# Kernel tuning notes

Hardware: AMD Instinct MI355X
Metric: run time of the kernel (lower is better)

## Reference

```python
import jax, jax.numpy as jnp
import numpy as np

EMBED_DIM = 1024
NUM_HEADS = 16
D_K = EMBED_DIM // NUM_HEADS
FFN_DIM = 4096
EPS = 1e-5


def _linear_params(key, fan_in, fan_out):
    kw, kb = jax.random.split(key)
    bound = 1.0 / np.sqrt(fan_in)
    W = jax.random.uniform(kw, (fan_out, fan_in), jnp.float32, -bound, bound)
    b = jax.random.uniform(kb, (fan_out,), jnp.float32, -bound, bound)
    return W, b


def setup_inputs() -> dict:
    key = jax.random.key(0)
    ks = jax.random.split(key, 8)
    x = jax.random.normal(ks[0], (2, 2048, EMBED_DIM), jnp.float32)
    Wq, bq = _linear_params(ks[1], EMBED_DIM, EMBED_DIM)
    Wk, bk = _linear_params(ks[2], EMBED_DIM, EMBED_DIM)
    Wv, bv = _linear_params(ks[3], EMBED_DIM, EMBED_DIM)
    Wo, bo = _linear_params(ks[4], EMBED_DIM, EMBED_DIM)
    W1, b1 = _linear_params(ks[5], EMBED_DIM, FFN_DIM)
    W2, b2 = _linear_params(ks[6], FFN_DIM, EMBED_DIM)
    g1 = jnp.ones((EMBED_DIM,), jnp.float32)
    be1 = jnp.zeros((EMBED_DIM,), jnp.float32)
    g2 = jnp.ones((EMBED_DIM,), jnp.float32)
    be2 = jnp.zeros((EMBED_DIM,), jnp.float32)
    return {"x": x, "Wq": Wq, "bq": bq, "Wk": Wk, "bk": bk, "Wv": Wv, "bv": bv,
            "Wo": Wo, "bo": bo, "W1": W1, "b1": b1, "W2": W2, "b2": b2,
            "g1": g1, "be1": be1, "g2": g2, "be2": be2}


def _layernorm(x, g, b):
    mu = jnp.mean(x, axis=-1, keepdims=True)
    var = jnp.var(x, axis=-1, keepdims=True)
    return (x - mu) * jax.lax.rsqrt(var + EPS) * g + b


def reference(x, Wq, bq, Wk, bk, Wv, bv, Wo, bo, W1, b1, W2, b2, g1, be1, g2, be2):
    B, S, _ = x.shape
    h = _layernorm(x, g1, be1)
    # qkv projections -> [B, H, S, d_k]
    def split_heads(t):
        return t.reshape(B, S, NUM_HEADS, D_K).transpose(0, 2, 1, 3)
    q = split_heads(h @ Wq.T + bq)
    k = split_heads(h @ Wk.T + bk)
    v = split_heads(h @ Wv.T + bv)
    scores = jnp.einsum('bhqd,bhkd->bhqk', q, k) / np.sqrt(D_K).astype(np.float32)
    attn = jax.nn.softmax(scores, axis=-1)
    out = jnp.einsum('bhqk,bhkd->bhqd', attn, v)
    out = out.transpose(0, 2, 1, 3).reshape(B, S, EMBED_DIM)
    attn_out = out @ Wo.T + bo
    x = x + attn_out
    h2 = _layernorm(x, g2, be2)
    ffn = jax.nn.relu(h2 @ W1.T + b1) @ W2.T + b2
    return x + ffn
```

## Files before the change

### kernel.cpp

```cpp
#include <hip/hip_runtime.h>

typedef __attribute__((ext_vector_type(8))) short short8;
typedef __attribute__((ext_vector_type(4))) float f32x4;
typedef __attribute__((ext_vector_type(4))) unsigned short us4;

#define MFMA_BF16(a, b, c) __builtin_amdgcn_mfma_f32_16x16x32_bf16((a), (b), (c), 0, 0, 0)

__device__ __forceinline__ unsigned short f2bf(float f) {
  union { float f; unsigned int u; } x; x.f = f;
  unsigned int r = x.u + 0x7FFFu + ((x.u >> 16) & 1u);
  return (unsigned short)(r >> 16);
}
__device__ __forceinline__ float bf2f(unsigned short b) {
  union { float f; unsigned int u; } x; x.u = ((unsigned int)b) << 16;
  return x.f;
}

typedef __attribute__((address_space(3))) unsigned int lds_uint;
typedef const __attribute__((address_space(1))) unsigned int gbl_uint;

__device__ __forceinline__ void gload_lds16(const void* g, void* l) {
  __builtin_amdgcn_global_load_lds((gbl_uint*)g, (lds_uint*)l, 16, 0, 0);
}

__device__ __forceinline__ short8 lds_swz_read(const unsigned short* base, int row, int colbyte) {
  return *(const short8*)((const char*)base + row * 128 + (colbyte ^ ((row & 7) << 4)));
}

__global__ __launch_bounds__(256) void cvt_ln(const float* __restrict__ Wq,
                                              const float* __restrict__ Wk,
                                              const float* __restrict__ Wv,
                                              const float* __restrict__ Wo,
                                              const float* __restrict__ W1,
                                              const float* __restrict__ W2,
                                              unsigned short* __restrict__ Wqkv_b,
                                              unsigned short* __restrict__ Wo_b,
                                              unsigned short* __restrict__ W1_b,
                                              unsigned short* __restrict__ W2_b,
                                              const float* __restrict__ x,
                                              const float* __restrict__ g,
                                              const float* __restrict__ be,
                                              unsigned short* __restrict__ lnout) {
  const int b = blockIdx.x;
  const int t = threadIdx.x;
  __shared__ float red[8];
  if (b < 12288) {
    const float* src;
    unsigned short* dst;
    int off;
    if (b < 1024)      { src = Wq; dst = Wqkv_b;           off = b; }
    else if (b < 2048) { src = Wk; dst = Wqkv_b + 1048576; off = b - 1024; }
    else if (b < 3072) { src = Wv; dst = Wqkv_b + 2097152; off = b - 2048; }
    else if (b < 4096) { src = Wo; dst = Wo_b;             off = b - 3072; }
    else if (b < 8192) { src = W1; dst = W1_b;             off = b - 4096; }
    else               { src = W2; dst = W2_b;             off = b - 8192; }
    const int i = off * 256 + t;
    const float4 v = ((const float4*)src)[i];
    us4 o;
    o.x = f2bf(v.x); o.y = f2bf(v.y); o.z = f2bf(v.z); o.w = f2bf(v.w);
    ((us4*)dst)[i] = o;
    return;
  }
  const int row = b - 12288;
  const float4 v = ((const float4*)(x + (size_t)row * 1024))[t];
  float s = v.x + v.y + v.z + v.w;
  float s2 = v.x * v.x + v.y * v.y + v.z * v.z + v.w * v.w;
#pragma unroll
  for (int d = 1; d < 64; d <<= 1) {
    s += __shfl_xor(s, d);
    s2 += __shfl_xor(s2, d);
  }
  const int wid = t >> 6, lane = t & 63;
  if (lane == 0) { red[wid] = s; red[4 + wid] = s2; }
  __syncthreads();
  s = red[0] + red[1] + red[2] + red[3];
  s2 = red[4] + red[5] + red[6] + red[7];
  const float mu = s * (1.0f / 1024.0f);
  const float var = s2 * (1.0f / 1024.0f) - mu * mu;
  const float rstd = rsqrtf(var + 1e-5f);
  const float4 gv = ((const float4*)g)[t];
  const float4 bv = ((const float4*)be)[t];
  us4 o;
  o.x = f2bf((v.x - mu) * rstd * gv.x + bv.x);
  o.y = f2bf((v.y - mu) * rstd * gv.y + bv.y);
  o.z = f2bf((v.z - mu) * rstd * gv.z + bv.z);
  o.w = f2bf((v.w - mu) * rstd * gv.w + bv.w);
  ((us4*)(lnout + (size_t)row * 1024))[t] = o;
}

__global__ __launch_bounds__(256) void ln_kernel(const float* __restrict__ x,
                                                 const float* __restrict__ g,
                                                 const float* __restrict__ be,
                                                 unsigned short* __restrict__ out) {
  const int row = blockIdx.x;
  const int t = threadIdx.x;
  const float4 v = ((const float4*)(x + (size_t)row * 1024))[t];
  float s = v.x + v.y + v.z + v.w;
  float s2 = v.x * v.x + v.y * v.y + v.z * v.z + v.w * v.w;
#pragma unroll
  for (int d = 1; d < 64; d <<= 1) {
    s += __shfl_xor(s, d);
    s2 += __shfl_xor(s2, d);
  }
  __shared__ float red[8];
  const int wid = t >> 6, lane = t & 63;
  if (lane == 0) { red[wid] = s; red[4 + wid] = s2; }
  __syncthreads();
  s = red[0] + red[1] + red[2] + red[3];
  s2 = red[4] + red[5] + red[6] + red[7];
  const float mu = s * (1.0f / 1024.0f);
  const float var = s2 * (1.0f / 1024.0f) - mu * mu;
  const float rstd = rsqrtf(var + 1e-5f);
  const float4 gv = ((const float4*)g)[t];
  const float4 bv = ((const float4*)be)[t];
  us4 o;
  o.x = f2bf((v.x - mu) * rstd * gv.x + bv.x);
  o.y = f2bf((v.y - mu) * rstd * gv.y + bv.y);
  o.z = f2bf((v.z - mu) * rstd * gv.z + bv.z);
  o.w = f2bf((v.w - mu) * rstd * gv.w + bv.w);
  ((us4*)(out + (size_t)row * 1024))[t] = o;
}

__global__ __launch_bounds__(256) void ffn2_reduce(float* __restrict__ out,
                                                   const float* __restrict__ p1,
                                                   const float* __restrict__ x1,
                                                   const float* __restrict__ b2) {
  const int row = blockIdx.x, t = threadIdx.x;
  const size_t i = (size_t)row * 256 + t;
  float4 v = ((const float4*)out)[i];
  const float4 a = ((const float4*)p1)[i];
  const float4 c = ((const float4*)x1)[i];
  const float4 b = ((const float4*)b2)[t];
  v.x += a.x + c.x + b.x; v.y += a.y + c.y + b.y;
  v.z += a.z + c.z + b.z; v.w += a.w + c.w + b.w;
  ((float4*)out)[i] = v;
}

template <int BN, int EPI, int MINW = 2>
__global__ __launch_bounds__(256, MINW) void gemm_bf16(const unsigned short* __restrict__ A,
                                                       const unsigned short* __restrict__ B,
                                                       const float* __restrict__ bias,
                                                       const float* __restrict__ biasK,
                                                       const float* __restrict__ biasV,
                                                       const float* __restrict__ res,
                                                       void* __restrict__ outp,
                                                       int M, int N, int K,
                                                       int gx, int gy, int kspl) {
  constexpr int WN = (BN == 128) ? 2 : 1;
  constexpr int WROWS = 128 / (4 / WN);
  constexpr int MW = WROWS / 16;
  constexpr int NW = (BN / WN) / 16;
  constexpr int BCH = BN / 32;
  constexpr int LOADS = 4 + BCH;

  __shared__ __align__(16) unsigned short As[2][128 * 64];
  __shared__ __align__(16) unsigned short Bs[2][BN * 64];

  const int nwg = gridDim.x;
  const int id2 = ((int)blockIdx.x & 7) * (nwg >> 3) + ((int)blockIdx.x >> 3);
  const int bx = id2 % gx;
  const int byz = id2 / gx;
  const int by = byz % gy;
  const int bz = byz / gy;

  const int wid = threadIdx.x >> 6;
  const int lane = threadIdx.x & 63;
  const int lr = lane & 15, lg = lane >> 4;
  const int row0 = by * 128;
  const int col0 = bx * BN;
  const int k0 = bz * kspl;
  const int wm = (wid / WN) * WROWS;
  const int wn = (wid % WN) * (BN / WN);

  const int scol = ((lane & 7) ^ ((lane >> 3) & 7)) * 8;

  auto stage = [&](int buf, int kt) {
#pragma unroll
    for (int i = 0; i < 4; ++i) {
      const int r = wid * 32 + i * 8;
      gload_lds16(A + (size_t)(row0 + r + (lane >> 3)) * K + kt + scol,
                  (void*)&As[buf][r * 64]);
    }
#pragma unroll
    for (int i = 0; i < BCH; ++i) {
      const int r = wid * (8 * BCH) + i * 8;
      gload_lds16(B + (size_t)(col0 + r + (lane >> 3)) * K + kt + scol,
                  (void*)&Bs[buf][r * 64]);
    }
  };

  f32x4 acc[MW][NW];
#pragma unroll
  for (int m = 0; m < MW; ++m)
#pragma unroll
    for (int n = 0; n < NW; ++n) acc[m][n] = (f32x4){0.f, 0.f, 0.f, 0.f};

  auto mma = [&](int buf) {
#pragma unroll
    for (int kk = 0; kk < 64; kk += 32) {
      const int colbyte = kk * 2 + lg * 16;
      short8 av[MW], bv[NW];
#pragma unroll
      for (int m = 0; m < MW; ++m)
        av[m] = lds_swz_read(&As[buf][0], wm + m * 16 + lr, colbyte);
#pragma unroll
      for (int n = 0; n < NW; ++n)
        bv[n] = lds_swz_read(&Bs[buf][0], wn + n * 16 + lr, colbyte);
#pragma unroll
      for (int m = 0; m < MW; ++m)
#pragma unroll
        for (int n = 0; n < NW; ++n) acc[m][n] = MFMA_BF16(av[m], bv[n], acc[m][n]);
    }
  };

  stage(0, k0);
  stage(1, k0 + 64);
  const int ktend = k0 + kspl;
  int cur = 0;
  for (int kt = k0; kt < ktend - 64; kt += 64) {
    asm volatile("s_waitcnt vmcnt(%0)" ::"i"(LOADS) : "memory");
    __builtin_amdgcn_s_barrier();
    __builtin_amdgcn_sched_barrier(0);
    mma(cur);
    __builtin_amdgcn_s_barrier();
    if (kt + 128 < ktend) stage(cur, kt + 128);
    cur ^= 1;
  }
  asm volatile("s_waitcnt vmcnt(0)" ::: "memory");
  __builtin_amdgcn_s_barrier();
  __builtin_amdgcn_sched_barrier(0);
  mma(cur);

#pragma unroll
  for (int m = 0; m < MW; ++m) {
#pragma unroll
    for (int n = 0; n < NW; ++n) {
#pragma unroll
      for (int r = 0; r < 4; ++r) {
        const int row = row0 + wm + m * 16 + lg * 4 + r;
        const int col = col0 + wn + n * 16 + lr;
        if constexpr (EPI == 0) {
          const int which = col >> 10, c = col & 1023;
          const float* bp = (which == 0) ? bias : (which == 1) ? biasK : biasV;
          const float v = acc[m][n][r] + bp[c];
          const size_t idx = (size_t)which * 4194304 +
              ((((size_t)(row >> 11)) * 16 + (c >> 6)) * 2048 + (row & 2047)) * 64 + (c & 63);
          ((unsigned short*)outp)[idx] = f2bf(v);
        } else if constexpr (EPI == 1) {
          const float v = acc[m][n][r] + bias[col];
          ((unsigned short*)outp)[(size_t)row * N + col] = f2bf(fmaxf(v, 0.f));
        } else {
          const float v = acc[m][n][r] + bias[col];
          ((float*)outp)[(size_t)row * N + col] = v + res[(size_t)row * N + col];
        }
      }
    }
  }
}

template <int BM, int BN, int EPI>
__global__ __launch_bounds__(512, 2) void gemm256(const unsigned short* __restrict__ A,
                                                  const unsigned short* __restrict__ B,
                                                  const float* __restrict__ bias,
                                                  float* __restrict__ part,
                                                  void* __restrict__ outp,
                                                  int M, int N, int K,
                                                  int gx, int gy, int kspl) {
  constexpr int MW = BM / 32;
  constexpr int NW = BN / 64;
  constexpr int A_ISS = BM / 64;
  constexpr int B_ISS = BN / 64;
  constexpr int LOADS = A_ISS + B_ISS;

  __shared__ __align__(16) unsigned short As[2][BM * 64];
  __shared__ __align__(16) unsigned short Bs[2][BN * 64];

  const int nwg = gridDim.x;
  const int id2 = ((int)blockIdx.x & 7) * (nwg >> 3) + ((int)blockIdx.x >> 3);
  const int bx = id2 % gx;
  const int byz = id2 / gx;
  const int by = byz % gy;
  const int bz = byz / gy;

  const int wid = threadIdx.x >> 6;
  const int lane = threadIdx.x & 63;
  const int lr = lane & 15, lg = lane >> 4;
  const int wr = wid >> 2, wc = wid & 3;
  const int row0 = by * BM;
  const int col0 = bx * BN;
  const int k0 = bz * kspl;
  const int wm = wr * (BM / 2);
  const int wn = wc * (BN / 4);

  const int scol = ((lane & 7) ^ ((lane >> 3) & 7)) * 8;

  auto stage = [&](int buf, int kt) {
#pragma unroll
    for (int i = 0; i < A_ISS; ++i) {
      const int r = wid * 8 + i * 64;
      gload_lds16(A + (size_t)(row0 + r + (lane >> 3)) * K + kt + scol,
                  (void*)&As[buf][r * 64]);
    }
#pragma unroll
    for (int i = 0; i < B_ISS; ++i) {
      const int r = wid * 8 + i * 64;
      gload_lds16(B + (size_t)(col0 + r + (lane >> 3)) * K + kt + scol,
                  (void*)&Bs[buf][r * 64]);
    }
  };

  f32x4 acc[MW][NW];
#pragma unroll
  for (int m = 0; m < MW; ++m)
#pragma unroll
    for (int n = 0; n < NW; ++n) acc[m][n] = (f32x4){0.f, 0.f, 0.f, 0.f};

  auto mma = [&](int buf) {
#pragma unroll
    for (int kk = 0; kk < 64; kk += 32) {
      const int colbyte = kk * 2 + lg * 16;
      short8 av[MW], bv[NW];
#pragma unroll
      for (int m = 0; m < MW; ++m)
        av[m] = lds_swz_read(&As[buf][0], wm + m * 16 + lr, colbyte);
#pragma unroll
      for (int n = 0; n < NW; ++n)
        bv[n] = lds_swz_read(&Bs[buf][0], wn + n * 16 + lr, colbyte);
#pragma unroll
      for (int m = 0; m < MW; ++m)
#pragma unroll
        for (int n = 0; n < NW; ++n) acc[m][n] = MFMA_BF16(av[m], bv[n], acc[m][n]);
    }
  };

  stage(0, k0);
  stage(1, k0 + 64);
  const int ktend = k0 + kspl;
  int cur = 0;
  for (int kt = k0; kt < ktend - 64; kt += 64) {
    asm volatile("s_waitcnt vmcnt(%0)" ::"i"(LOADS) : "memory");
    __builtin_amdgcn_s_barrier();
    __builtin_amdgcn_sched_barrier(0);
    mma(cur);
    __builtin_amdgcn_s_barrier();
    if (kt + 128 < ktend) stage(cur, kt + 128);
    cur ^= 1;
  }
  asm volatile("s_waitcnt vmcnt(0)" ::: "memory");
  __builtin_amdgcn_s_barrier();
  __builtin_amdgcn_sched_barrier(0);
  mma(cur);

#pragma unroll
  for (int m = 0; m < MW; ++m) {
#pragma unroll
    for (int n = 0; n < NW; ++n) {
#pragma unroll
      for (int r = 0; r < 4; ++r) {
        const int row = row0 + wm + m * 16 + lg * 4 + r;
        const int col = col0 + wn + n * 16 + lr;
        if constexpr (EPI == 1) {
          const float v = acc[m][n][r] + bias[col];
          ((unsigned short*)outp)[(size_t)row * N + col] = f2bf(fmaxf(v, 0.f));
        } else {
          float* dst = bz ? part : (float*)outp;
          dst[(size_t)row * N + col] = acc[m][n][r];
        }
      }
    }
  }
}

__global__ __launch_bounds__(256, 2) void attn_kernel(const unsigned short* __restrict__ q,
                                                      const unsigned short* __restrict__ k,
                                                      const unsigned short* __restrict__ v,
                                                      unsigned short* __restrict__ o) {
  const int bh = blockIdx.x;
  const int q0 = blockIdx.y * 128;
  const unsigned short* qh = q + (size_t)bh * 2048 * 64;
  const unsigned short* kh = k + (size_t)bh * 2048 * 64;
  const unsigned short* vh = v + (size_t)bh * 2048 * 64;
  const int wid = threadIdx.x >> 6, lane = threadIdx.x & 63;
  const int lr = lane & 15, lg = lane >> 4;
  const int qw = q0 + wid * 32;

  __shared__ __align__(16) unsigned short Vt[2][64 * 64];
  __shared__ __align__(16) unsigned short Ps[4][32 * 64];

  constexpr float CS = 0.125f * 1.4426950408889634f;
  short8 qf[2][2];
#pragma unroll
  for (int m = 0; m < 2; ++m)
#pragma unroll
    for (int kk = 0; kk < 2; ++kk) {
      short8 t = *(const short8*)&qh[(size_t)(qw + m * 16 + lr) * 64 + kk * 32 + lg * 8];
#pragma unroll
      for (int j = 0; j < 8; ++j) t[j] = (short)f2bf(bf2f((unsigned short)t[j]) * CS);
      qf[m][kk] = t;
    }

  f32x4 po[2][4];
  float lrun[2][4];
#pragma unroll
  for (int m = 0; m < 2; ++m) {
#pragma unroll
    for (int n = 0; n < 4; ++n) po[m][n] = (f32x4){0.f, 0.f, 0.f, 0.f};
#pragma unroll
    for (int r = 0; r < 4; ++r) lrun[m][r] = 0.f;
  }

  const int vd0 = wid * 16;
  const unsigned short* const vsrc = vh + (size_t)lane * 64 + vd0;
  const int sig2 = ((lane & 15) << 3) | ((lane >> 4) << 1);
  char* const PsB = (char*)&Ps[wid][0];

  short8 kfA[4][2], kfB[4][2], vA0, vA1, vB0, vB1;

#define LOAD_K(KF, kt)                                                                   \
  {                                                                                      \
    _Pragma("unroll") for (int n = 0; n < 4; ++n) _Pragma("unroll") for (int kk = 0;     \
                                                                         kk < 2; ++kk)  \
        KF[n][kk] =                                                                      \
        *(const short8*)&kh[(size_t)((kt) + n * 16 + lr) * 64 + kk * 32 + lg * 8];       \
  }
#define LOAD_V(V0, V1, kt)                                                               \
  {                                                                                      \
    V0 = *(const short8*)(vsrc + (size_t)(kt) * 64);                                     \
    V1 = *(const short8*)(vsrc + (size_t)(kt) * 64 + 8);                                 \
  }

  LOAD_K(kfA, 0)
  LOAD_V(vA0, vA1, 0)

#define STEP(KC, KN, VC0, VC1, VN0, VN1, BUF, t)                                         \
  {                                                                                      \
    char* const VtB = (char*)&Vt[BUF][0];                                                \
    _Pragma("unroll") for (int j = 0; j < 8; ++j) {                                      \
      const int row = vd0 + j;                                                           \
      *(unsigned short*)(VtB + row * 128 + (sig2 ^ ((row & 7) << 4))) =                  \
          (unsigned short)VC0[j];                                                        \
      const int row2 = vd0 + 8 + j;                                                      \
      *(unsigned short*)(VtB + row2 * 128 + (sig2 ^ ((row2 & 7) << 4))) =                \
          (unsigned short)VC1[j];                                                        \
    }                                                                                    \
    f32x4 sc[2][4];                                                                      \
    _Pragma("unroll") for (int m = 0; m < 2; ++m) _Pragma("unroll") for (int n = 0;      \
                                                                         n < 4; ++n)    \
        sc[m][n] = (f32x4){0.f, 0.f, 0.f, 0.f};                                          \
    __builtin_amdgcn_s_setprio(1);                                                       \
    _Pragma("unroll") for (int kk = 0; kk < 2; ++kk)                                     \
        _Pragma("unroll") for (int m = 0; m < 2; ++m)                                    \
        _Pragma("unroll") for (int n = 0; n < 4; ++n)                                    \
        sc[m][n] = MFMA_BF16(qf[m][kk], KC[n][kk], sc[m][n]);                            \
    __builtin_amdgcn_s_setprio(0);                                                       \
    const int ktn = ((t) + 1 < 32) ? ((t) + 1) * 64 : 0;                                 \
    LOAD_V(VN0, VN1, ktn)                                                                \
    LOAD_K(KN, ktn)                                                                      \
    _Pragma("unroll") for (int m = 0; m < 2; ++m)                                        \
        _Pragma("unroll") for (int r = 0; r < 4; ++r) {                                  \
      const float p0 = __builtin_amdgcn_exp2f(sc[m][0][r]);                              \
      const float p1 = __builtin_amdgcn_exp2f(sc[m][1][r]);                              \
      const float p2 = __builtin_amdgcn_exp2f(sc[m][2][r]);                              \
      const float p3 = __builtin_amdgcn_exp2f(sc[m][3][r]);                              \
      lrun[m][r] += (p0 + p1) + (p2 + p3);                                               \
      unsigned int u0, u1;                                                               \
      asm("v_cvt_pk_bf16_f32 %0, %1, %2" : "=v"(u0) : "v"(p0), "v"(p1));                 \
      asm("v_cvt_pk_bf16_f32 %0, %1, %2" : "=v"(u1) : "v"(p2), "v"(p3));                 \
      const int row = m * 16 + lg * 4 + r;                                               \
      uint2 pk2; pk2.x = u0; pk2.y = u1;                                                 \
      *(uint2*)(PsB + row * 128 + ((lr * 8) ^ ((row & 7) << 4))) = pk2;                  \
    }                                                                                    \
    asm volatile("s_waitcnt lgkmcnt(0)" ::: "memory");                                   \
    __builtin_amdgcn_s_barrier();                                                        \
    __builtin_amdgcn_sched_barrier(0);                                                   \
    _Pragma("unroll") for (int kk = 0; kk < 2; ++kk) {                                   \
      const int coff = kk * 64 + lg * 16;                                                \
      short8 pa[2], vbr[4];                                                              \
      _Pragma("unroll") for (int m = 0; m < 2; ++m) {                                    \
        const int prow = m * 16 + lr;                                                    \
        pa[m] = *(const short8*)(PsB + prow * 128 + (coff ^ ((prow & 7) << 4)));         \
      }                                                                                  \
      _Pragma("unroll") for (int n = 0; n < 4; ++n) {                                    \
        const int vrow = n * 16 + lr;                                                    \
        vbr[n] = *(const short8*)(VtB + vrow * 128 + (coff ^ ((vrow & 7) << 4)));        \
      }                                                                                  \
      __builtin_amdgcn_s_setprio(1);                                                     \
      _Pragma("unroll") for (int m = 0; m < 2; ++m)                                      \
          _Pragma("unroll") for (int n = 0; n < 4; ++n)                                  \
          po[m][n] = MFMA_BF16(pa[m], vbr[n], po[m][n]);                                 \
      __builtin_amdgcn_s_setprio(0);                                                     \
    }                                                                                    \
  }

  for (int t = 0; t < 32; t += 2) {
    STEP(kfA, kfB, vA0, vA1, vB0, vB1, 0, t)
    STEP(kfB, kfA, vB0, vB1, vA0, vA1, 1, t + 1)
  }
#undef STEP
#undef LOAD_K
#undef LOAD_V

#pragma unroll
  for (int d = 1; d < 16; d <<= 1)
#pragma unroll
    for (int m = 0; m < 2; ++m)
#pragma unroll
      for (int r = 0; r < 4; ++r) lrun[m][r] += __shfl_xor(lrun[m][r], d);

  const int b = bh >> 4, hh = bh & 15;
#pragma unroll
  for (int m = 0; m < 2; ++m)
#pragma unroll
    for (int n = 0; n < 4; ++n)
#pragma unroll
      for (int r = 0; r < 4; ++r) {
        const int qrow = qw + m * 16 + lg * 4 + r;
        const int d = n * 16 + lr;
        o[((size_t)b * 2048 + qrow) * 1024 + hh * 64 + d] =
            f2bf(po[m][n][r] / lrun[m][r]);
      }
}

extern "C" void kernel_launch(void* const* d_in, const int* in_sizes, int n_in,
                              void* d_out, int out_size, void* d_ws, size_t ws_size,
                              hipStream_t stream) {
  const float* x  = (const float*)d_in[0];
  const float* Wq = (const float*)d_in[1];
  const float* bq = (const float*)d_in[2];
  const float* Wk = (const float*)d_in[3];
  const float* bk = (const float*)d_in[4];
  const float* Wv = (const float*)d_in[5];
  const float* bv = (const float*)d_in[6];
  const float* Wo = (const float*)d_in[7];
  const float* bo = (const float*)d_in[8];
  const float* W1 = (const float*)d_in[9];
  const float* b1 = (const float*)d_in[10];
  const float* W2 = (const float*)d_in[11];
  const float* b2 = (const float*)d_in[12];
  const float* g1 = (const float*)d_in[13];
  const float* be1 = (const float*)d_in[14];
  const float* g2 = (const float*)d_in[15];
  const float* be2 = (const float*)d_in[16];

  char* ws = (char*)d_ws;
  const size_t MB = 1024 * 1024;
  unsigned short* Wqkv_b = (unsigned short*)(ws + 0 * MB);
  unsigned short* Wo_b   = (unsigned short*)(ws + 6 * MB);
  unsigned short* W1_b   = (unsigned short*)(ws + 8 * MB);
  unsigned short* W2_b   = (unsigned short*)(ws + 16 * MB);
  unsigned short* h_b    = (unsigned short*)(ws + 24 * MB);
  unsigned short* qb     = (unsigned short*)(ws + 32 * MB);
  unsigned short* ab     = (unsigned short*)(ws + 56 * MB);
  float*          x1     = (float*)(ws + 64 * MB);
  unsigned short* fb     = (unsigned short*)(ws + 32 * MB);
  float*          p1     = (float*)(ws + 0 * MB);

  cvt_ln<<<16384, 256, 0, stream>>>(Wq, Wk, Wv, Wo, W1, W2, Wqkv_b, Wo_b, W1_b, W2_b,
                                    x, g1, be1, h_b);

  gemm_bf16<128, 0><<<768, 256, 0, stream>>>(h_b, Wqkv_b, bq, bk, bv, nullptr, qb,
                                             4096, 3072, 1024, 24, 32, 1024);

  attn_kernel<<<dim3(32, 16), 256, 0, stream>>>(qb, qb + 4194304, qb + 2 * 4194304, ab);

  gemm_bf16<64, 2, 3><<<512, 256, 0, stream>>>(ab, Wo_b, bo, nullptr, nullptr, x, x1,
                                               4096, 1024, 1024, 16, 32, 1024);

  ln_kernel<<<4096, 256, 0, stream>>>(x1, g2, be2, h_b);

  gemm256<256, 256, 1><<<256, 512, 0, stream>>>(h_b, W1_b, b1, nullptr, fb,
                                                4096, 4096, 1024, 16, 16, 1024);

  gemm256<128, 256, 4><<<256, 512, 0, stream>>>(fb, W2_b, nullptr, p1, (float*)d_out,
                                                4096, 1024, 4096, 4, 32, 2048);

  ffn2_reduce<<<4096, 256, 0, stream>>>((float*)d_out, p1, x1, b2);
}
```

Baseline: 248.1 us.

## Emit V pre-transposed for async LDS staging and store FFN2 split-K partials as bf16

The QKV GEMM epilogue now writes V in a transposed, swizzled [d][seq] layout. The attention kernel can then stage V tiles straight into LDS with global_load_lds into a double buffer, instead of loading V to registers and scattering 16-bit transposed writes to LDS each step. Separately, the FFN2 split-K GEMM writes both partials as bf16 into workspace, and the reduce kernel converts them back and adds the residual and bias, which halves partial-sum traffic. The trade-offs are rounding of fp32 partial sums to bf16, and a more scattered epilogue store pattern for V.

```diff
diff --git a/kernel.cpp b/kernel.cpp
--- a/kernel.cpp
+++ b/kernel.cpp
@@ -122,17 +122,21 @@
 }
 
 __global__ __launch_bounds__(256) void ffn2_reduce(float* __restrict__ out,
-                                                   const float* __restrict__ p1,
+                                                   const unsigned short* __restrict__ p0,
+                                                   const unsigned short* __restrict__ p1,
                                                    const float* __restrict__ x1,
                                                    const float* __restrict__ b2) {
   const int row = blockIdx.x, t = threadIdx.x;
   const size_t i = (size_t)row * 256 + t;
-  float4 v = ((const float4*)out)[i];
-  const float4 a = ((const float4*)p1)[i];
+  const us4 a0 = ((const us4*)p0)[i];
+  const us4 a1 = ((const us4*)p1)[i];
   const float4 c = ((const float4*)x1)[i];
   const float4 b = ((const float4*)b2)[t];
-  v.x += a.x + c.x + b.x; v.y += a.y + c.y + b.y;
-  v.z += a.z + c.z + b.z; v.w += a.w + c.w + b.w;
+  float4 v;
+  v.x = bf2f(a0.x) + bf2f(a1.x) + c.x + b.x;
+  v.y = bf2f(a0.y) + bf2f(a1.y) + c.y + b.y;
+  v.z = bf2f(a0.z) + bf2f(a1.z) + c.z + b.z;
+  v.w = bf2f(a0.w) + bf2f(a1.w) + c.w + b.w;
   ((float4*)out)[i] = v;
 }
 
@@ -243,9 +247,18 @@
           const int which = col >> 10, c = col & 1023;
           const float* bp = (which == 0) ? bias : (which == 1) ? biasK : biasV;
           const float v = acc[m][n][r] + bp[c];
-          const size_t idx = (size_t)which * 4194304 +
-              ((((size_t)(row >> 11)) * 16 + (c >> 6)) * 2048 + (row & 2047)) * 64 + (c & 63);
-          ((unsigned short*)outp)[idx] = f2bf(v);
+          const unsigned short b16 = f2bf(v);
+          const int bb = row >> 11, sl = row & 2047;
+          if (which < 2) {
+            const size_t idx = (size_t)which * 4194304 +
+                (((size_t)bb * 16 + (c >> 6)) * 2048 + sl) * 64 + (c & 63);
+            ((unsigned short*)outp)[idx] = b16;
+          } else {
+            const int sig = ((sl & 15) << 2) | ((sl >> 4) & 3);
+            const size_t idx = (size_t)2 * 4194304 +
+                (((size_t)bb * 16 + (c >> 6)) * 64 + (c & 63)) * 2048 + (sl & ~63) + sig;
+            ((unsigned short*)outp)[idx] = b16;
+          }
         } else if constexpr (EPI == 1) {
           const float v = acc[m][n][r] + bias[col];
           ((unsigned short*)outp)[(size_t)row * N + col] = f2bf(fmaxf(v, 0.f));
@@ -262,7 +275,7 @@
 __global__ __launch_bounds__(512, 2) void gemm256(const unsigned short* __restrict__ A,
                                                   const unsigned short* __restrict__ B,
                                                   const float* __restrict__ bias,
-                                                  float* __restrict__ part,
+                                                  void* __restrict__ part,
                                                   void* __restrict__ outp,
                                                   int M, int N, int K,
                                                   int gx, int gy, int kspl) {
@@ -363,8 +376,8 @@
           const float v = acc[m][n][r] + bias[col];
           ((unsigned short*)outp)[(size_t)row * N + col] = f2bf(fmaxf(v, 0.f));
         } else {
-          float* dst = bz ? part : (float*)outp;
-          dst[(size_t)row * N + col] = acc[m][n][r];
+          unsigned short* dst = (unsigned short*)(bz ? part : outp);
+          dst[(size_t)row * N + col] = f2bf(acc[m][n][r]);
         }
       }
     }
@@ -373,13 +386,13 @@
 
 __global__ __launch_bounds__(256, 2) void attn_kernel(const unsigned short* __restrict__ q,
                                                       const unsigned short* __restrict__ k,
-                                                      const unsigned short* __restrict__ v,
+                                                      const unsigned short* __restrict__ vt,
                                                       unsigned short* __restrict__ o) {
   const int bh = blockIdx.x;
   const int q0 = blockIdx.y * 128;
   const unsigned short* qh = q + (size_t)bh * 2048 * 64;
   const unsigned short* kh = k + (size_t)bh * 2048 * 64;
-  const unsigned short* vh = v + (size_t)bh * 2048 * 64;
+  const unsigned short* vh = vt + (size_t)bh * 64 * 2048;
   const int wid = threadIdx.x >> 6, lane = threadIdx.x & 63;
   const int lr = lane & 15, lg = lane >> 4;
   const int qw = q0 + wid * 32;
@@ -409,12 +422,10 @@
     for (int r = 0; r < 4; ++r) lrun[m][r] = 0.f;
   }
 
-  const int vd0 = wid * 16;
-  const unsigned short* const vsrc = vh + (size_t)lane * 64 + vd0;
-  const int sig2 = ((lane & 15) << 3) | ((lane >> 4) << 1);
+  const int scol = ((lane & 7) ^ ((lane >> 3) & 7)) * 8;
   char* const PsB = (char*)&Ps[wid][0];
 
-  short8 kfA[4][2], kfB[4][2], vA0, vA1, vB0, vB1;
+  short8 kfA[4][2], kfB[4][2];
 
 #define LOAD_K(KF, kt)                                                                   \
   {                                                                                      \
@@ -423,26 +434,20 @@
         KF[n][kk] =                                                                      \
         *(const short8*)&kh[(size_t)((kt) + n * 16 + lr) * 64 + kk * 32 + lg * 8];       \
   }
-#define LOAD_V(V0, V1, kt)                                                               \
+#define STAGE_VT(BUF, kt)                                                                \
   {                                                                                      \
-    V0 = *(const short8*)(vsrc + (size_t)(kt) * 64);                                     \
-    V1 = *(const short8*)(vsrc + (size_t)(kt) * 64 + 8);                                 \
+    _Pragma("unroll") for (int i = 0; i < 2; ++i) {                                      \
+      const int r = (wid * 2 + i) * 8;                                                   \
+      gload_lds16(vh + (size_t)(r + (lane >> 3)) * 2048 + (kt) + scol,                   \
+                  (void*)&Vt[BUF][r * 64]);                                              \
+    }                                                                                    \
   }
 
   LOAD_K(kfA, 0)
-  LOAD_V(vA0, vA1, 0)
-
-#define STEP(KC, KN, VC0, VC1, VN0, VN1, BUF, t)                                         \
+  STAGE_VT(0, 0)
+
+#define STEP(KC, KN, BUF, t)                                                             \
   {                                                                                      \
-    char* const VtB = (char*)&Vt[BUF][0];                                                \
-    _Pragma("unroll") for (int j = 0; j < 8; ++j) {                                      \
-      const int row = vd0 + j;                                                           \
-      *(unsigned short*)(VtB + row * 128 + (sig2 ^ ((row & 7) << 4))) =                  \
-          (unsigned short)VC0[j];                                                        \
-      const int row2 = vd0 + 8 + j;                                                      \
-      *(unsigned short*)(VtB + row2 * 128 + (sig2 ^ ((row2 & 7) << 4))) =                \
-          (unsigned short)VC1[j];                                                        \
-    }                                                                                    \
     f32x4 sc[2][4];                                                                      \
     _Pragma("unroll") for (int m = 0; m < 2; ++m) _Pragma("unroll") for (int n = 0;      \
                                                                          n < 4; ++n)    \
@@ -454,7 +459,6 @@
         sc[m][n] = MFMA_BF16(qf[m][kk], KC[n][kk], sc[m][n]);                            \
     __builtin_amdgcn_s_setprio(0);                                                       \
     const int ktn = ((t) + 1 < 32) ? ((t) + 1) * 64 : 0;                                 \
-    LOAD_V(VN0, VN1, ktn)                                                                \
     LOAD_K(KN, ktn)                                                                      \
     _Pragma("unroll") for (int m = 0; m < 2; ++m)                                        \
         _Pragma("unroll") for (int r = 0; r < 4; ++r) {                                  \
@@ -470,8 +474,11 @@
       uint2 pk2; pk2.x = u0; pk2.y = u1;                                                 \
       *(uint2*)(PsB + row * 128 + ((lr * 8) ^ ((row & 7) << 4))) = pk2;                  \
     }                                                                                    \
-    asm volatile("s_waitcnt lgkmcnt(0)" ::: "memory");                                   \
+               \
+    asm volatile("s_waitcnt vmcnt(8) lgkmcnt(0)" ::: "memory");                          \
     __builtin_amdgcn_s_barrier();                                                        \
+    __builtin_amdgcn_sched_barrier(0);                                                   \
+    STAGE_VT(BUF ^ 1, ktn)          \
     __builtin_amdgcn_sched_barrier(0);                                                   \
     _Pragma("unroll") for (int kk = 0; kk < 2; ++kk) {                                   \
       const int coff = kk * 64 + lg * 16;                                                \
@@ -480,10 +487,8 @@
         const int prow = m * 16 + lr;                                                    \
         pa[m] = *(const short8*)(PsB + prow * 128 + (coff ^ ((prow & 7) << 4)));         \
       }                                                                                  \
-      _Pragma("unroll") for (int n = 0; n < 4; ++n) {                                    \
-        const int vrow = n * 16 + lr;                                                    \
-        vbr[n] = *(const short8*)(VtB + vrow * 128 + (coff ^ ((vrow & 7) << 4)));        \
-      }                                                                                  \
+      _Pragma("unroll") for (int n = 0; n < 4; ++n)                                      \
+        vbr[n] = lds_swz_read(&Vt[BUF][0], n * 16 + lr, coff);                           \
       __builtin_amdgcn_s_setprio(1);                                                     \
       _Pragma("unroll") for (int m = 0; m < 2; ++m)                                      \
           _Pragma("unroll") for (int n = 0; n < 4; ++n)                                  \
@@ -493,12 +498,12 @@
   }
 
   for (int t = 0; t < 32; t += 2) {
-    STEP(kfA, kfB, vA0, vA1, vB0, vB1, 0, t)
-    STEP(kfB, kfA, vB0, vB1, vA0, vA1, 1, t + 1)
+    STEP(kfA, kfB, 0, t)
+    STEP(kfB, kfA, 1, t + 1)
   }
 #undef STEP
 #undef LOAD_K
-#undef LOAD_V
+#undef STAGE_VT
 
 #pragma unroll
   for (int d = 1; d < 16; d <<= 1)
@@ -553,7 +558,8 @@
   unsigned short* ab     = (unsigned short*)(ws + 56 * MB);
   float*          x1     = (float*)(ws + 64 * MB);
   unsigned short* fb     = (unsigned short*)(ws + 32 * MB);
-  float*          p1     = (float*)(ws + 0 * MB);
+  unsigned short* p0     = (unsigned short*)(ws + 0 * MB);
+  unsigned short* p1     = (unsigned short*)(ws + 8 * MB);
 
   cvt_ln<<<16384, 256, 0, stream>>>(Wq, Wk, Wv, Wo, W1, W2, Wqkv_b, Wo_b, W1_b, W2_b,
                                     x, g1, be1, h_b);
@@ -571,8 +577,8 @@
   gemm256<256, 256, 1><<<256, 512, 0, stream>>>(h_b, W1_b, b1, nullptr, fb,
                                                 4096, 4096, 1024, 16, 16, 1024);
 
-  gemm256<128, 256, 4><<<256, 512, 0, stream>>>(fb, W2_b, nullptr, p1, (float*)d_out,
+  gemm256<128, 256, 4><<<256, 512, 0, stream>>>(fb, W2_b, nullptr, p1, p0,
                                                 4096, 1024, 4096, 4, 32, 2048);
 
-  ffn2_reduce<<<4096, 256, 0, stream>>>((float*)d_out, p1, x1, b2);
-}
+  ffn2_reduce<<<4096, 256, 0, stream>>>((float*)d_out, p0, p1, x1, b2);
+}
```

After: 256.1 us. 3.2% more time.
